# Optimization experiments

Hardware: AMD Instinct MI355X
Metric: run time of the kernel (lower is better)

## Reference

```python
import jax, jax.numpy as jnp
import numpy as np

N, L, D = 512, 40, 128      # batch, peptide length, embedding dim
O, K, MHC = 256, 9, 34      # out_channels, kernel_size, mhc_len
STRIDE = 1


def setup_inputs() -> dict:
    key = jax.random.key(0)
    k1, k2, k3 = jax.random.split(key, 3)
    peptide_x = jax.random.normal(k1, (N, L, D), dtype=jnp.float32)
    mhc_x = jax.random.normal(k2, (N, MHC, D), dtype=jnp.float32)
    weight = jax.random.normal(k3, (O, K, MHC), dtype=jnp.float32) * 0.02  # truncated_normal std=0.02 approx
    bias = jnp.zeros((O,), dtype=jnp.float32)
    return {"peptide_x": peptide_x, "mhc_x": mhc_x, "weight": weight, "bias": bias}


def reference(peptide_x, mhc_x, weight, bias):
    # Per-sample dynamic kernel generation: [n, O, d, K]
    kernel = jax.nn.relu(jnp.einsum('nld,okl->nodk', mhc_x, weight))
    k = weight.shape[1]
    T = (peptide_x.shape[1] - k) // STRIDE + 1  # conv1d output length
    # Sliding windows of the peptide: [n, T, K, d]
    idx = jnp.arange(T)[:, None] * STRIDE + jnp.arange(k)[None, :]
    win = peptide_x[:, idx, :]
    # Grouped (groups=batch) conv1d as a batched contraction: [n, O, T]
    out = jnp.einsum('ntkd,nodk->not', win, kernel) + bias[None, :, None]
    return out
```

## Files before the change

kernel.cpp:

```cpp
#include <hip/hip_runtime.h>
#include <hip/hip_bf16.h>

typedef unsigned short u16;
typedef unsigned int u32;
typedef __bf16 bf16x8 __attribute__((ext_vector_type(8)));
typedef float f32x4 __attribute__((ext_vector_type(4)));
typedef unsigned int u32x4 __attribute__((ext_vector_type(4)));
typedef unsigned int u32x2 __attribute__((ext_vector_type(2)));

#define NN 512
#define LL 40
#define DD 128
#define OO 256
#define KK 9
#define MHCL 34
#define TT 32
#define PSTR 136
#define KDSTR 72
#define WPADL 64

#define PEPT_U16 (LL * PSTR)
#define KS_U16   (32 * KDSTR)
#define EX_U16   2048

__device__ __forceinline__ u16 f2bf(float x) {
    unsigned int u = __builtin_bit_cast(unsigned int, x);
    u = (u + 0x7FFFu + ((u >> 16) & 1u)) >> 16;
    return (u16)u;
}
__device__ __forceinline__ u32 pk2(float a, float b) {
    __hip_bfloat162 h = __float22bfloat162_rn(make_float2(a, b));
    u32 r;
    __builtin_memcpy(&r, &h, 4);
    return r;
}
__device__ __forceinline__ bf16x8 ld8(const u16* p) {
    u32x4 r;
    __builtin_memcpy(&r, __builtin_assume_aligned(p, 16), 16);
    return __builtin_bit_cast(bf16x8, r);
}
__device__ __forceinline__ f32x4 mfma16(bf16x8 a, bf16x8 b, f32x4 c) {
    return __builtin_amdgcn_mfma_f32_16x16x32_bf16(a, b, c, 0, 0, 0);
}

__global__ void cvt_all(const float* __restrict__ wgt, const float* __restrict__ pept,
                        u32* __restrict__ wp, u32* __restrict__ pp) {
    int i = blockIdx.x * 256 + threadIdx.x;
    const int WN = OO * KK * (WPADL / 2);
    if (i < WN) {
        int o = i / (KK * (WPADL / 2));
        int r = i - o * (KK * (WPADL / 2));
        int k = r >> 5;
        int lp = (r & 31) << 1;
        const float* src = wgt + ((size_t)o * KK + k) * MHCL;
        float a = (lp     < MHCL) ? src[lp]     : 0.f;
        float b = (lp + 1 < MHCL) ? src[lp + 1] : 0.f;
        wp[i] = pk2(a, b);
    } else {
        size_t j = (size_t)(i - WN);
        if (j < (size_t)NN * LL * DD / 2)
            pp[j] = pk2(pept[2 * j], pept[2 * j + 1]);
    }
}

__global__ __launch_bounds__(256, 2)
void iconv_fast(const float* __restrict__ mhc,
                const u16* __restrict__ wp,
                const u16* __restrict__ pb,
                const float* __restrict__ bias,
                float* __restrict__ out)
{
    __shared__ __align__(16) u16 s_mem[PEPT_U16 + 2 * EX_U16];

    const int tid  = threadIdx.x;
    const int wave = tid >> 6;
    const int pair = wave >> 1;
    const int dh   = wave & 1;
    const int lane = tid & 63;
    const int quad = lane >> 4;
    const int l16  = lane & 15;

    const int n  = blockIdx.x >> 2;
    const int oq = blockIdx.x & 3;
    const int obase = (oq * 2 + pair) * 32;

    u16* const s_pept = s_mem;

    auto loadW = [&](int o_base, int k, bf16x8 wF[2][2]) {
        #pragma unroll
        for (int mt = 0; mt < 2; ++mt) {
            const u16* wr = wp + ((size_t)(o_base + mt * 16 + l16) * KK + k) * WPADL;
            u32x4 r0, r1;
            __builtin_memcpy(&r0, __builtin_assume_aligned(wr + quad * 8, 16), 16);
            __builtin_memcpy(&r1, __builtin_assume_aligned(wr + 32 + quad * 8, 16), 16);
            wF[mt][0] = __builtin_bit_cast(bf16x8, r0);
            wF[mt][1] = __builtin_bit_cast(bf16x8, r1);
        }
    };

    bf16x8 wB[2][2];
    loadW(obase, 0, wB);

    bf16x8 mA[4][2];
    {
        const float* mg = mhc + (size_t)n * MHCL * DD;
        #pragma unroll
        for (int di = 0; di < 4; ++di) {
            const int d = dh * 64 + 32 * (di & 1) + 8 * (l16 >> 2) + 4 * (di >> 1) + (l16 & 3);
            u16 h0[8];
            #pragma unroll
            for (int j = 0; j < 8; ++j)
                h0[j] = f2bf(mg[(size_t)(quad * 8 + j) * DD + d]);
            __builtin_memcpy(&mA[di][0], h0, 16);
            u16 h1[8] = {0,0,0,0,0,0,0,0};
            if (quad == 0) {
                h1[0] = f2bf(mg[(size_t)32 * DD + d]);
                h1[1] = f2bf(mg[(size_t)33 * DD + d]);
            }
            __builtin_memcpy(&mA[di][1], h1, 16);
        }
    }

    {
        const u16* pg = pb + (size_t)n * LL * DD;
        #pragma unroll 1
        for (int i = tid; i < (LL * DD) / 8; i += 256) {
            int row = i >> 4, c8 = (i & 15) << 3;
            u32x4 v;
            __builtin_memcpy(&v, __builtin_assume_aligned(pg + (size_t)row * DD + c8, 16), 16);
            __builtin_memcpy(__builtin_assume_aligned(&s_pept[row * PSTR + c8], 16), &v, 16);
        }
    }
    __syncthreads();

    f32x4 acc00 = {0.f,0.f,0.f,0.f}, acc01 = acc00, acc10 = acc00, acc11 = acc00;

    #pragma unroll 3
    for (int k = 0; k < KK; ++k) {
        u32x2 kc0[4], kc1[4];
        #pragma unroll
        for (int di = 0; di < 4; ++di) {
            f32x4 c0 = {0.f,0.f,0.f,0.f}, c1 = c0;
            c0 = mfma16(mA[di][0], wB[0][0], c0);
            c0 = mfma16(mA[di][1], wB[0][1], c0);
            c1 = mfma16(mA[di][0], wB[1][0], c1);
            c1 = mfma16(mA[di][1], wB[1][1], c1);
            kc0[di][0] = pk2(fmaxf(c0[0], 0.f), fmaxf(c0[1], 0.f));
            kc0[di][1] = pk2(fmaxf(c0[2], 0.f), fmaxf(c0[3], 0.f));
            kc1[di][0] = pk2(fmaxf(c1[0], 0.f), fmaxf(c1[1], 0.f));
            kc1[di][1] = pk2(fmaxf(c1[2], 0.f), fmaxf(c1[3], 0.f));
        }
        if (k < KK - 1) loadW(obase, k + 1, wB);
        #pragma unroll
        for (int ds = 0; ds < 2; ++ds) {
            u32x4 b0 = { kc0[ds][0], kc0[ds][1], kc0[ds + 2][0], kc0[ds + 2][1] };
            u32x4 b1 = { kc1[ds][0], kc1[ds][1], kc1[ds + 2][0], kc1[ds + 2][1] };
            bf16x8 bk0 = __builtin_bit_cast(bf16x8, b0);
            bf16x8 bk1 = __builtin_bit_cast(bf16x8, b1);
            bf16x8 ap0 = ld8(&s_pept[(k + l16) * PSTR + dh * 64 + ds * 32 + quad * 8]);
            bf16x8 ap1 = ld8(&s_pept[(k + 16 + l16) * PSTR + dh * 64 + ds * 32 + quad * 8]);
            acc00 = mfma16(ap0, bk0, acc00);
            acc01 = mfma16(ap0, bk1, acc01);
            acc10 = mfma16(ap1, bk0, acc10);
            acc11 = mfma16(ap1, bk1, acc11);
        }
    }

    if (dh == 1) {
        float* ox = (float*)(s_mem + PEPT_U16 + pair * EX_U16);
        const int fb = lane * 16;
        __builtin_memcpy(__builtin_assume_aligned(&ox[fb +  0], 16), &acc00, 16);
        __builtin_memcpy(__builtin_assume_aligned(&ox[fb +  4], 16), &acc01, 16);
        __builtin_memcpy(__builtin_assume_aligned(&ox[fb +  8], 16), &acc10, 16);
        __builtin_memcpy(__builtin_assume_aligned(&ox[fb + 12], 16), &acc11, 16);
    }
    __syncthreads();
    if (dh == 0) {
        const float* px = (const float*)(s_mem + PEPT_U16 + pair * EX_U16);
        const int fb = lane * 16;
        f32x4 q00, q01, q10, q11;
        __builtin_memcpy(&q00, __builtin_assume_aligned(&px[fb +  0], 16), 16);
        __builtin_memcpy(&q01, __builtin_assume_aligned(&px[fb +  4], 16), 16);
        __builtin_memcpy(&q10, __builtin_assume_aligned(&px[fb +  8], 16), 16);
        __builtin_memcpy(&q11, __builtin_assume_aligned(&px[fb + 12], 16), 16);
        const float bv0 = bias[obase + l16];
        const float bv1 = bias[obase + 16 + l16];
        f32x4 r00 = acc00 + q00 + bv0;
        f32x4 r01 = acc01 + q01 + bv1;
        f32x4 r10 = acc10 + q10 + bv0;
        f32x4 r11 = acc11 + q11 + bv1;
        float* ob = out + ((size_t)n * OO + obase) * TT;
        __builtin_memcpy(__builtin_assume_aligned(ob + (size_t)l16 * TT + quad * 4, 16), &r00, 16);
        __builtin_memcpy(__builtin_assume_aligned(ob + (size_t)(16 + l16) * TT + quad * 4, 16), &r01, 16);
        __builtin_memcpy(__builtin_assume_aligned(ob + (size_t)l16 * TT + 16 + quad * 4, 16), &r10, 16);
        __builtin_memcpy(__builtin_assume_aligned(ob + (size_t)(16 + l16) * TT + 16 + quad * 4, 16), &r11, 16);
    }
}

__global__ __launch_bounds__(256, 2)
void iconv_ref(const float* __restrict__ pept,
               const float* __restrict__ mhc,
               const float* __restrict__ wgt,
               const float* __restrict__ bias,
               float* __restrict__ out)
{
    __shared__ __align__(16) u16 s_mem[PEPT_U16 + 4 * KS_U16];
    const int tid  = threadIdx.x;
    const int wave = tid >> 6;
    const int dh   = wave & 1;
    const int lane = tid & 63;
    const int quad = lane >> 4;
    const int l16  = lane & 15;
    const int n  = blockIdx.x >> 2;
    const int oq = blockIdx.x & 3;
    const int obase = (oq * 2 + (wave >> 1)) * 32;
    u16* const s_pept = s_mem;
    u16* const ks     = s_mem + PEPT_U16 + wave * KS_U16;

    auto loadW = [&](int o_base, int k, bf16x8 wF[2][2]) {
        #pragma unroll
        for (int mt = 0; mt < 2; ++mt) {
            const float* wrow = wgt + ((size_t)(o_base + mt * 16 + l16) * KK + k) * MHCL;
            float w8[8];
            __builtin_memcpy(w8, __builtin_assume_aligned(wrow + quad * 8, 8), 32);
            u16 h0[8];
            #pragma unroll
            for (int j = 0; j < 8; ++j) h0[j] = f2bf(w8[j]);
            __builtin_memcpy(&wF[mt][0], h0, 16);
            u16 h1[8] = {0,0,0,0,0,0,0,0};
            if (quad == 0) { h1[0] = f2bf(wrow[32]); h1[1] = f2bf(wrow[33]); }
            __builtin_memcpy(&wF[mt][1], h1, 16);
        }
    };

    bf16x8 wB[2][2];
    loadW(obase, 0, wB);

    bf16x8 mA[4][2];
    {
        const float* mg = mhc + (size_t)n * MHCL * DD;
        #pragma unroll
        for (int di = 0; di < 4; ++di) {
            const int d = dh * 64 + di * 16 + l16;
            u16 h0[8];
            #pragma unroll
            for (int j = 0; j < 8; ++j)
                h0[j] = f2bf(mg[(size_t)(quad * 8 + j) * DD + d]);
            __builtin_memcpy(&mA[di][0], h0, 16);
            u16 h1[8] = {0,0,0,0,0,0,0,0};
            if (quad == 0) {
                h1[0] = f2bf(mg[(size_t)32 * DD + d]);
                h1[1] = f2bf(mg[(size_t)33 * DD + d]);
            }
            __builtin_memcpy(&mA[di][1], h1, 16);
        }
    }

    {
        const float* pg = pept + (size_t)n * LL * DD;
        #pragma unroll 1
        for (int i = tid; i < (LL * DD) / 4; i += 256) {
            int row = i >> 5, c4 = (i & 31) << 2;
            f32x4 v;
            __builtin_memcpy(&v, __builtin_assume_aligned(pg + row * DD + c4, 16), 16);
            u32x2 h = { pk2(v[0], v[1]), pk2(v[2], v[3]) };
            __builtin_memcpy(__builtin_assume_aligned(&s_pept[row * PSTR + c4], 8), &h, 8);
        }
    }
    __syncthreads();

    f32x4 acc00 = {0.f,0.f,0.f,0.f}, acc01 = acc00, acc10 = acc00, acc11 = acc00;

    #pragma unroll 3
    for (int k = 0; k < KK; ++k) {
        #pragma unroll
        for (int di = 0; di < 4; ++di) {
            f32x4 c0 = {0.f,0.f,0.f,0.f}, c1 = c0;
            c0 = mfma16(mA[di][0], wB[0][0], c0);
            c0 = mfma16(mA[di][1], wB[0][1], c0);
            c1 = mfma16(mA[di][0], wB[1][0], c1);
            c1 = mfma16(mA[di][1], wB[1][1], c1);
            u32x2 p0 = { pk2(fmaxf(c0[0], 0.f), fmaxf(c0[1], 0.f)),
                         pk2(fmaxf(c0[2], 0.f), fmaxf(c0[3], 0.f)) };
            u32x2 p1 = { pk2(fmaxf(c1[0], 0.f), fmaxf(c1[1], 0.f)),
                         pk2(fmaxf(c1[2], 0.f), fmaxf(c1[3], 0.f)) };
            __builtin_memcpy(__builtin_assume_aligned(&ks[l16 * KDSTR + di * 16 + quad * 4], 8), &p0, 8);
            __builtin_memcpy(__builtin_assume_aligned(&ks[(16 + l16) * KDSTR + di * 16 + quad * 4], 8), &p1, 8);
        }
        if (k < KK - 1) loadW(obase, k + 1, wB);
        #pragma unroll
        for (int ds = 0; ds < 2; ++ds) {
            bf16x8 kb0 = ld8(&ks[l16 * KDSTR + ds * 32 + quad * 8]);
            bf16x8 kb1 = ld8(&ks[(16 + l16) * KDSTR + ds * 32 + quad * 8]);
            bf16x8 ap0 = ld8(&s_pept[(k + l16) * PSTR + dh * 64 + ds * 32 + quad * 8]);
            bf16x8 ap1 = ld8(&s_pept[(k + 16 + l16) * PSTR + dh * 64 + ds * 32 + quad * 8]);
            acc00 = mfma16(ap0, kb0, acc00);
            acc01 = mfma16(ap0, kb1, acc01);
            acc10 = mfma16(ap1, kb0, acc10);
            acc11 = mfma16(ap1, kb1, acc11);
        }
    }

    if (dh == 1) {
        float* ox = (float*)ks;
        const int fb = lane * 16;
        __builtin_memcpy(__builtin_assume_aligned(&ox[fb +  0], 16), &acc00, 16);
        __builtin_memcpy(__builtin_assume_aligned(&ox[fb +  4], 16), &acc01, 16);
        __builtin_memcpy(__builtin_assume_aligned(&ox[fb +  8], 16), &acc10, 16);
        __builtin_memcpy(__builtin_assume_aligned(&ox[fb + 12], 16), &acc11, 16);
    }
    __syncthreads();
    if (dh == 0) {
        const float* px = (const float*)(s_mem + PEPT_U16 + (wave + 1) * KS_U16);
        const int fb = lane * 16;
        f32x4 q00, q01, q10, q11;
        __builtin_memcpy(&q00, __builtin_assume_aligned(&px[fb +  0], 16), 16);
        __builtin_memcpy(&q01, __builtin_assume_aligned(&px[fb +  4], 16), 16);
        __builtin_memcpy(&q10, __builtin_assume_aligned(&px[fb +  8], 16), 16);
        __builtin_memcpy(&q11, __builtin_assume_aligned(&px[fb + 12], 16), 16);
        const float bv0 = bias[obase + l16];
        const float bv1 = bias[obase + 16 + l16];
        f32x4 r00 = acc00 + q00 + bv0;
        f32x4 r01 = acc01 + q01 + bv1;
        f32x4 r10 = acc10 + q10 + bv0;
        f32x4 r11 = acc11 + q11 + bv1;
        float* ob = out + ((size_t)n * OO + obase) * TT;
        __builtin_memcpy(__builtin_assume_aligned(ob + (size_t)l16 * TT + quad * 4, 16), &r00, 16);
        __builtin_memcpy(__builtin_assume_aligned(ob + (size_t)(16 + l16) * TT + quad * 4, 16), &r01, 16);
        __builtin_memcpy(__builtin_assume_aligned(ob + (size_t)l16 * TT + 16 + quad * 4, 16), &r10, 16);
        __builtin_memcpy(__builtin_assume_aligned(ob + (size_t)(16 + l16) * TT + 16 + quad * 4, 16), &r11, 16);
    }
}

extern "C" void kernel_launch(void* const* d_in, const int* in_sizes, int n_in,
                              void* d_out, int out_size, void* d_ws, size_t ws_size,
                              hipStream_t stream) {
    const float* pept = (const float*)d_in[0];
    const float* mhc  = (const float*)d_in[1];
    const float* wgt  = (const float*)d_in[2];
    const float* bias = (const float*)d_in[3];
    float* out = (float*)d_out;

    const size_t w_bytes = (size_t)OO * KK * WPADL * sizeof(u16);
    const size_t p_bytes = (size_t)NN * LL * DD * sizeof(u16);
    if (ws_size >= w_bytes + p_bytes) {
        u16* wp = (u16*)d_ws;
        u16* pp = (u16*)((char*)d_ws + w_bytes);
        const int total = OO * KK * (WPADL / 2) + NN * LL * DD / 2;
        cvt_all<<<dim3((total + 255) / 256), dim3(256), 0, stream>>>(wgt, pept, (u32*)wp, (u32*)pp);
        iconv_fast<<<dim3(NN * 4), dim3(256), 0, stream>>>(mhc, wp, pp, bias, out);
    } else {
        iconv_ref<<<dim3(NN * 4), dim3(256), 0, stream>>>(pept, mhc, wgt, bias, out);
    }
}
```

Baseline: 116.7 us.

## Split D across four waves with 16 channels per block to raise occupancy

After: 146.8 us. 25.8% more time.

```diff
diff --git a/kernel.cpp b/kernel.cpp
--- a/kernel.cpp
+++ b/kernel.cpp
@@ -21,7 +21,7 @@
 
 #define PEPT_U16 (LL * PSTR)
 #define KS_U16   (32 * KDSTR)
-#define EX_U16   2048
+#define EX_U16   1024
 
 __device__ __forceinline__ u16 f2bf(float x) {
     unsigned int u = __builtin_bit_cast(unsigned int, x);
@@ -63,50 +63,45 @@
     }
 }
 
-__global__ __launch_bounds__(256, 2)
+__global__ __launch_bounds__(256, 8)
 void iconv_fast(const float* __restrict__ mhc,
                 const u16* __restrict__ wp,
                 const u16* __restrict__ pb,
                 const float* __restrict__ bias,
                 float* __restrict__ out)
 {
-    __shared__ __align__(16) u16 s_mem[PEPT_U16 + 2 * EX_U16];
+    __shared__ __align__(16) u16 s_mem[PEPT_U16 + 3 * EX_U16];
 
     const int tid  = threadIdx.x;
-    const int wave = tid >> 6;
-    const int pair = wave >> 1;
-    const int dh   = wave & 1;
+    const int dq   = tid >> 6;
     const int lane = tid & 63;
     const int quad = lane >> 4;
     const int l16  = lane & 15;
 
-    const int n  = blockIdx.x >> 2;
-    const int oq = blockIdx.x & 3;
-    const int obase = (oq * 2 + pair) * 32;
+    const int n  = blockIdx.x >> 4;
+    const int oc = blockIdx.x & 15;
+    const int obase = oc * 16;
 
     u16* const s_pept = s_mem;
 
-    auto loadW = [&](int o_base, int k, bf16x8 wF[2][2]) {
-        #pragma unroll
-        for (int mt = 0; mt < 2; ++mt) {
-            const u16* wr = wp + ((size_t)(o_base + mt * 16 + l16) * KK + k) * WPADL;
-            u32x4 r0, r1;
-            __builtin_memcpy(&r0, __builtin_assume_aligned(wr + quad * 8, 16), 16);
-            __builtin_memcpy(&r1, __builtin_assume_aligned(wr + 32 + quad * 8, 16), 16);
-            wF[mt][0] = __builtin_bit_cast(bf16x8, r0);
-            wF[mt][1] = __builtin_bit_cast(bf16x8, r1);
-        }
+    auto loadW = [&](int k, bf16x8 wF[2]) {
+        const u16* wr = wp + ((size_t)(obase + l16) * KK + k) * WPADL;
+        u32x4 r0, r1;
+        __builtin_memcpy(&r0, __builtin_assume_aligned(wr + quad * 8, 16), 16);
+        __builtin_memcpy(&r1, __builtin_assume_aligned(wr + 32 + quad * 8, 16), 16);
+        wF[0] = __builtin_bit_cast(bf16x8, r0);
+        wF[1] = __builtin_bit_cast(bf16x8, r1);
     };
 
-    bf16x8 wB[2][2];
-    loadW(obase, 0, wB);
-
-    bf16x8 mA[4][2];
+    bf16x8 wB[2];
+    loadW(0, wB);
+
+    bf16x8 mA[2][2];
     {
         const float* mg = mhc + (size_t)n * MHCL * DD;
         #pragma unroll
-        for (int di = 0; di < 4; ++di) {
-            const int d = dh * 64 + 32 * (di & 1) + 8 * (l16 >> 2) + 4 * (di >> 1) + (l16 & 3);
+        for (int di = 0; di < 2; ++di) {
+            const int d = dq * 32 + 8 * (l16 >> 2) + 4 * di + (l16 & 3);
             u16 h0[8];
             #pragma unroll
             for (int j = 0; j < 8; ++j)
@@ -133,67 +128,52 @@
     }
     __syncthreads();
 
-    f32x4 acc00 = {0.f,0.f,0.f,0.f}, acc01 = acc00, acc10 = acc00, acc11 = acc00;
+    f32x4 acc00 = {0.f,0.f,0.f,0.f}, acc10 = acc00;
 
     #pragma unroll 3
     for (int k = 0; k < KK; ++k) {
-        u32x2 kc0[4], kc1[4];
-        #pragma unroll
-        for (int di = 0; di < 4; ++di) {
-            f32x4 c0 = {0.f,0.f,0.f,0.f}, c1 = c0;
-            c0 = mfma16(mA[di][0], wB[0][0], c0);
-            c0 = mfma16(mA[di][1], wB[0][1], c0);
-            c1 = mfma16(mA[di][0], wB[1][0], c1);
-            c1 = mfma16(mA[di][1], wB[1][1], c1);
-            kc0[di][0] = pk2(fmaxf(c0[0], 0.f), fmaxf(c0[1], 0.f));
-            kc0[di][1] = pk2(fmaxf(c0[2], 0.f), fmaxf(c0[3], 0.f));
-            kc1[di][0] = pk2(fmaxf(c1[0], 0.f), fmaxf(c1[1], 0.f));
-            kc1[di][1] = pk2(fmaxf(c1[2], 0.f), fmaxf(c1[3], 0.f));
-        }
-        if (k < KK - 1) loadW(obase, k + 1, wB);
-        #pragma unroll
-        for (int ds = 0; ds < 2; ++ds) {
-            u32x4 b0 = { kc0[ds][0], kc0[ds][1], kc0[ds + 2][0], kc0[ds + 2][1] };
-            u32x4 b1 = { kc1[ds][0], kc1[ds][1], kc1[ds + 2][0], kc1[ds + 2][1] };
-            bf16x8 bk0 = __builtin_bit_cast(bf16x8, b0);
-            bf16x8 bk1 = __builtin_bit_cast(bf16x8, b1);
-            bf16x8 ap0 = ld8(&s_pept[(k + l16) * PSTR + dh * 64 + ds * 32 + quad * 8]);
-            bf16x8 ap1 = ld8(&s_pept[(k + 16 + l16) * PSTR + dh * 64 + ds * 32 + quad * 8]);
-            acc00 = mfma16(ap0, bk0, acc00);
-            acc01 = mfma16(ap0, bk1, acc01);
-            acc10 = mfma16(ap1, bk0, acc10);
-            acc11 = mfma16(ap1, bk1, acc11);
-        }
-    }
-
-    if (dh == 1) {
-        float* ox = (float*)(s_mem + PEPT_U16 + pair * EX_U16);
-        const int fb = lane * 16;
-        __builtin_memcpy(__builtin_assume_aligned(&ox[fb +  0], 16), &acc00, 16);
-        __builtin_memcpy(__builtin_assume_aligned(&ox[fb +  4], 16), &acc01, 16);
-        __builtin_memcpy(__builtin_assume_aligned(&ox[fb +  8], 16), &acc10, 16);
-        __builtin_memcpy(__builtin_assume_aligned(&ox[fb + 12], 16), &acc11, 16);
+        u32x2 kc[2];
+        #pragma unroll
+        for (int di = 0; di < 2; ++di) {
+            f32x4 c0 = {0.f,0.f,0.f,0.f};
+            c0 = mfma16(mA[di][0], wB[0], c0);
+            c0 = mfma16(mA[di][1], wB[1], c0);
+            kc[di][0] = pk2(fmaxf(c0[0], 0.f), fmaxf(c0[1], 0.f));
+            kc[di][1] = pk2(fmaxf(c0[2], 0.f), fmaxf(c0[3], 0.f));
+        }
+        if (k < KK - 1) loadW(k + 1, wB);
+        u32x4 b0 = { kc[0][0], kc[0][1], kc[1][0], kc[1][1] };
+        bf16x8 bk0 = __builtin_bit_cast(bf16x8, b0);
+        bf16x8 ap0 = ld8(&s_pept[(k + l16) * PSTR + dq * 32 + quad * 8]);
+        bf16x8 ap1 = ld8(&s_pept[(k + 16 + l16) * PSTR + dq * 32 + quad * 8]);
+        acc00 = mfma16(ap0, bk0, acc00);
+        acc10 = mfma16(ap1, bk0, acc10);
+    }
+
+    if (dq != 0) {
+        float* ox = (float*)(s_mem + PEPT_U16 + (dq - 1) * EX_U16);
+        const int fb = lane * 8;
+        __builtin_memcpy(__builtin_assume_aligned(&ox[fb + 0], 16), &acc00, 16);
+        __builtin_memcpy(__builtin_assume_aligned(&ox[fb + 4], 16), &acc10, 16);
     }
     __syncthreads();
-    if (dh == 0) {
-        const float* px = (const float*)(s_mem + PEPT_U16 + pair * EX_U16);
-        const int fb = lane * 16;
-        f32x4 q00, q01, q10, q11;
-        __builtin_memcpy(&q00, __builtin_assume_aligned(&px[fb +  0], 16), 16);
-        __builtin_memcpy(&q01, __builtin_assume_aligned(&px[fb +  4], 16), 16);
-        __builtin_memcpy(&q10, __builtin_assume_aligned(&px[fb +  8], 16), 16);
-        __builtin_memcpy(&q11, __builtin_assume_aligned(&px[fb + 12], 16), 16);
-        const float bv0 = bias[obase + l16];
-        const float bv1 = bias[obase + 16 + l16];
-        f32x4 r00 = acc00 + q00 + bv0;
-        f32x4 r01 = acc01 + q01 + bv1;
-        f32x4 r10 = acc10 + q10 + bv0;
-        f32x4 r11 = acc11 + q11 + bv1;
+    if (dq == 0) {
+        const int fb = lane * 8;
+        #pragma unroll
+        for (int w = 0; w < 3; ++w) {
+            const float* px = (const float*)(s_mem + PEPT_U16 + w * EX_U16);
+            f32x4 q0, q1;
+            __builtin_memcpy(&q0, __builtin_assume_aligned(&px[fb + 0], 16), 16);
+            __builtin_memcpy(&q1, __builtin_assume_aligned(&px[fb + 4], 16), 16);
+            acc00 += q0;
+            acc10 += q1;
+        }
+        const float bv = bias[obase + l16];
+        f32x4 r00 = acc00 + bv;
+        f32x4 r10 = acc10 + bv;
         float* ob = out + ((size_t)n * OO + obase) * TT;
         __builtin_memcpy(__builtin_assume_aligned(ob + (size_t)l16 * TT + quad * 4, 16), &r00, 16);
-        __builtin_memcpy(__builtin_assume_aligned(ob + (size_t)(16 + l16) * TT + quad * 4, 16), &r01, 16);
         __builtin_memcpy(__builtin_assume_aligned(ob + (size_t)l16 * TT + 16 + quad * 4, 16), &r10, 16);
-        __builtin_memcpy(__builtin_assume_aligned(ob + (size_t)(16 + l16) * TT + 16 + quad * 4, 16), &r11, 16);
     }
 }
 
@@ -348,7 +328,7 @@
         u16* pp = (u16*)((char*)d_ws + w_bytes);
         const int total = OO * KK * (WPADL / 2) + NN * LL * DD / 2;
         cvt_all<<<dim3((total + 255) / 256), dim3(256), 0, stream>>>(wgt, pept, (u32*)wp, (u32*)pp);
-        iconv_fast<<<dim3(NN * 4), dim3(256), 0, stream>>>(mhc, wp, pp, bias, out);
+        iconv_fast<<<dim3(NN * 16), dim3(256), 0, stream>>>(mhc, wp, pp, bias, out);
     } else {
         iconv_ref<<<dim3(NN * 4), dim3(256), 0, stream>>>(pept, mhc, wgt, bias, out);
     }
```
